# Kernel tuning notes

Measured on AMD Instinct MI355X. Metric: run time of the kernel, lower is better.

## Reference

```python
import jax, jax.numpy as jnp
import numpy as np

NEG_SLOPE = 0.2  # PyG GATConv default leaky_relu slope
H1, F1 = 4, 64


def gat_layer(x, src, dst, n, W, a_src, a_dst, b, heads, out_dim, concat):
    # Linear transform then split heads: [N, H, F]
    h = (x @ W).reshape(n, heads, out_dim)
    # Per-node attention logits for source/destination roles: [N, H]
    e_src = jnp.sum(h * a_src, axis=-1)
    e_dst = jnp.sum(h * a_dst, axis=-1)
    # Per-edge score, LeakyReLU: [E, H]
    e = e_src[src] + e_dst[dst]
    e = jnp.where(e > 0, e, NEG_SLOPE * e)
    # Segment softmax over incoming edges of each destination node
    m = jax.ops.segment_max(e, dst, num_segments=n)  # [N, H]
    e = jnp.exp(e - jax.lax.stop_gradient(m)[dst])
    denom = jax.ops.segment_sum(e, dst, num_segments=n)  # [N, H]
    alpha = e / denom[dst]  # [E, H]
    # Scatter-aggregate weighted source features: [N, H, F]
    out = jax.ops.segment_sum(alpha[:, :, None] * h[src], dst, num_segments=n)
    if concat:
        out = out.reshape(n, heads * out_dim)
    else:
        out = out.mean(axis=1)
    return out + b


def setup_inputs() -> dict:
    key = jax.random.key(0)
    ks = jax.random.split(key, 16)
    N, E, D_IN, HID, C = 30000, 480000, 5000, 64, 3
    s = 0.05
    inp = {
        "x": jax.random.normal(ks[0], (N, D_IN), dtype=jnp.float32),
        "W1": jax.random.normal(ks[1], (D_IN, H1 * HID), dtype=jnp.float32) * s,
        "a1_src": jax.random.normal(ks[2], (H1, HID), dtype=jnp.float32) * s,
        "a1_dst": jax.random.normal(ks[3], (H1, HID), dtype=jnp.float32) * s,
        "b1": jnp.zeros((H1 * HID,), dtype=jnp.float32),
        "W2": jax.random.normal(ks[4], (H1 * HID, H1 * HID), dtype=jnp.float32) * s,
        "a2_src": jax.random.normal(ks[5], (H1, HID), dtype=jnp.float32) * s,
        "a2_dst": jax.random.normal(ks[6], (H1, HID), dtype=jnp.float32) * s,
        "b2": jnp.zeros((H1 * HID,), dtype=jnp.float32),
        "W3": jax.random.normal(ks[7], (H1 * HID, HID), dtype=jnp.float32) * s,
        "a3_src": jax.random.normal(ks[8], (1, HID), dtype=jnp.float32) * s,
        "a3_dst": jax.random.normal(ks[9], (1, HID), dtype=jnp.float32) * s,
        "b3": jnp.zeros((HID,), dtype=jnp.float32),
        "Wc": jax.random.normal(ks[10], (HID, C), dtype=jnp.float32) * s,
        "bc": jnp.zeros((C,), dtype=jnp.float32),
        "edge_index": jax.random.randint(ks[11], (2, E), 0, N, dtype=jnp.int64)
        if jax.config.jax_enable_x64
        else jax.random.randint(ks[11], (2, E), 0, N, dtype=jnp.int32),
    }
    return inp


def reference(x, W1, a1_src, a1_dst, b1, W2, a2_src, a2_dst, b2,
              W3, a3_src, a3_dst, b3, Wc, bc, edge_index):
    n = x.shape[0]
    loops = jnp.arange(n, dtype=edge_index.dtype)
    src = jnp.concatenate([edge_index[0], loops])  # add self-loops (PyG default)
    dst = jnp.concatenate([edge_index[1], loops])
    h = gat_layer(x, src, dst, n, W1, a1_src, a1_dst, b1, H1, F1, True)
    h = jax.nn.elu(h)
    h = gat_layer(h, src, dst, n, W2, a2_src, a2_dst, b2, H1, F1, True)
    h = jax.nn.elu(h)
    h = gat_layer(h, src, dst, n, W3, a3_src, a3_dst, b3, 1, F1, False)
    h = jax.nn.elu(h)
    return h @ Wc + bc
```

## Files before the change

### kernel.cpp

```cpp
#include <hip/hip_runtime.h>
#include <hip/hip_bf16.h>
#include <cstdint>
#include <cstddef>

typedef unsigned short u16;
typedef __attribute__((ext_vector_type(8))) short short8;
typedef __attribute__((ext_vector_type(4))) float f4;


__device__ __forceinline__ u16 f2bf(float x) {
    union { float f; uint32_t u; } v; v.f = x;
    uint32_t r = v.u + 0x7fffu + ((v.u >> 16) & 1u);
    return (u16)(r >> 16);
}

__device__ __forceinline__ void async16(const u16* g, u16* l) {
    __builtin_amdgcn_global_load_lds((__attribute__((address_space(1))) void*)(g),
                                     (__attribute__((address_space(3))) void*)(l),
                                     16, 0, 0);
}


template<int BM, int BN, int WM, int WN>
__global__ __launch_bounds__((BM/WM)*(BN/WN)*64)
void gemm_xw(const float* __restrict__ A, const u16* __restrict__ Bt,
             float* __restrict__ C, int M, int K, int KT, int ktPer)
{
    constexpr int WAVES   = (BM/WM)*(BN/WN);
    constexpr int THREADS = WAVES*64;
    constexpr int RF = WM/16, CF = WN/16;
    constexpr int BCH = (BN*64)/(16*THREADS);
    static_assert((BM*32)/THREADS == 8, "A staging assumes 8 floats per thread");

    __shared__ __align__(16) u16 As[BM*32];
    __shared__ __align__(16) u16 Bs[BN*32];

    const int tid  = threadIdx.x;
    const int wid  = tid >> 6, lane = tid & 63;
    const int quad = lane >> 4, l16 = lane & 15;
    constexpr int WCOLS = BN/WN;
    const int wm = (wid / WCOLS) * WM;
    const int wn = (wid % WCOLS) * WN;
    const long m0 = (long)blockIdx.x * BM;

    const int ktA = blockIdx.y * ktPer;
    const int ktB = min(ktA + ktPer, KT);
    float* Cp = C + (size_t)blockIdx.y * (size_t)M * BN;

    const int arow = tid >> 2;
    const int akk  = (tid & 3) * 8;
    const bool aok = (m0 + arow) < M;
    const float* aptr = A + (size_t)(m0 + arow) * K + akk;

    f4 acc[RF][CF];
    #pragma unroll
    for (int r = 0; r < RF; ++r)
        #pragma unroll
        for (int c = 0; c < CF; ++c)
            #pragma unroll
            for (int g = 0; g < 4; ++g) acc[r][c][g] = 0.f;

    const u16* Asl = As + (wm + l16)*32 + quad*8;
    const u16* Bsl = Bs + (wn + l16)*32 + quad*8;

    for (int kt = ktA; kt < ktB; ++kt) {
        __syncthreads();
        #pragma unroll
        for (int i = 0; i < BCH; ++i) {
            int c16 = i*THREADS + tid;
            async16(Bt + (size_t)kt*(BN*32) + (size_t)c16*8, (u16*)Bs + c16*8);
        }
        {
            const int gk = kt*32 + akk;
            f4 v0, v1;
            #pragma unroll
            for (int g = 0; g < 4; ++g) { v0[g] = 0.f; v1[g] = 0.f; }
            if (aok && gk < K) {
                const float* p = aptr + (size_t)kt*32;
                v0 = *(const f4*)p;
                v1 = *(const f4*)(p + 4);
            }
            short8 w;
            #pragma unroll
            for (int g = 0; g < 4; ++g) {
                w[g]   = (short)f2bf(v0[g]);
                w[4+g] = (short)f2bf(v1[g]);
            }
            *(short8*)(As + tid*8) = w;
        }
        __syncthreads();

        short8 af[RF], bfr[CF];
        #pragma unroll
        for (int r = 0; r < RF; ++r) af[r]  = *(const short8*)(Asl + r*16*32);
        #pragma unroll
        for (int c = 0; c < CF; ++c) bfr[c] = *(const short8*)(Bsl + c*16*32);
        #pragma unroll
        for (int r = 0; r < RF; ++r)
            #pragma unroll
            for (int c = 0; c < CF; ++c)
                acc[r][c] = __builtin_amdgcn_mfma_f32_16x16x32_bf16(af[r], bfr[c], acc[r][c], 0, 0, 0);
    }

    #pragma unroll
    for (int r = 0; r < RF; ++r) {
        const long rb = m0 + wm + r*16 + quad*4;
        #pragma unroll
        for (int c = 0; c < CF; ++c) {
            const int col = wn + c*16 + l16;
            #pragma unroll
            for (int g = 0; g < 4; ++g) {
                long row = rb + g;
                if (row < M) Cp[row*(long)BN + col] = acc[r][c][g];
            }
        }
    }
}

__global__ void k_reduce_scores(const float* __restrict__ parts, size_t partStride, int S,
                                const float* __restrict__ asrc, const float* __restrict__ adst,
                                float* __restrict__ h, float* __restrict__ es,
                                float* __restrict__ ed, int N)
{
    int wave = threadIdx.x >> 6, lane = threadIdx.x & 63;
    int node = blockIdx.x*4 + wave;
    if (node >= N) return;
    size_t base = (size_t)node*256 + lane*4;
    f4 v;
    #pragma unroll
    for (int g = 0; g < 4; ++g) v[g] = 0.f;
    for (int s = 0; s < S; ++s) {
        f4 p = *(const f4*)(parts + s*partStride + base);
        #pragma unroll
        for (int g = 0; g < 4; ++g) v[g] += p[g];
    }
    *(f4*)(h + base) = v;

    int hh = lane >> 4;
    int c0 = (lane & 15) * 4;
    float s = 0.f, d = 0.f;
    #pragma unroll
    for (int g = 0; g < 4; ++g) {
        s += v[g] * asrc[hh*64 + c0 + g];
        d += v[g] * adst[hh*64 + c0 + g];
    }
    #pragma unroll
    for (int off = 1; off < 16; off <<= 1) {
        s += __shfl_xor(s, off);
        d += __shfl_xor(d, off);
    }
    if ((lane & 15) == 0) { es[node*4 + hh] = s; ed[node*4 + hh] = d; }
}

__global__ void k_prep_w(const float* __restrict__ W, u16* __restrict__ out,
                         int K, int Nn, int total)
{
    int idx = blockIdx.x*256 + threadIdx.x;
    if (idx >= total) return;
    int ki = idx & 31;
    int rest = idx >> 5;
    int nn = rest % Nn;
    int kt = rest / Nn;
    int k = kt*32 + ki;
    float v = (k < K) ? W[(size_t)k*Nn + nn] : 0.f;
    out[idx] = f2bf(v);
}

__global__ void k_hist(const int* __restrict__ ei, int E, int N, int* counts)
{
    int i = blockIdx.x*256 + threadIdx.x;
    if (i >= E + N) return;
    int d = (i < E) ? ei[E + i] : (i - E);
    atomicAdd(&counts[d], 1);
}

__global__ void k_scan1(const int* __restrict__ counts, int* offs, int* partials, int N)
{
    __shared__ int s[256];
    int i = blockIdx.x*256 + threadIdx.x;
    int v = (i < N) ? counts[i] : 0;
    s[threadIdx.x] = v;
    __syncthreads();
    #pragma unroll
    for (int off = 1; off < 256; off <<= 1) {
        int t = (threadIdx.x >= off) ? s[threadIdx.x - off] : 0;
        __syncthreads();
        s[threadIdx.x] += t;
        __syncthreads();
    }
    if (i < N) offs[i + 1] = s[threadIdx.x];
    if (threadIdx.x == 255) partials[blockIdx.x] = s[255];
    if (i == 0) offs[0] = 0;
}

__global__ void k_scan2(int* partials, int NB)
{
    __shared__ int s[256];
    int v = (threadIdx.x < NB) ? partials[threadIdx.x] : 0;
    s[threadIdx.x] = v;
    __syncthreads();
    for (int off = 1; off < 256; off <<= 1) {
        int t = (threadIdx.x >= off) ? s[threadIdx.x - off] : 0;
        __syncthreads();
        s[threadIdx.x] += t;
        __syncthreads();
    }
    if (threadIdx.x < NB) partials[threadIdx.x] = s[threadIdx.x] - v;
}

__global__ void k_scan3(int* offs, const int* __restrict__ partials, int N)
{
    int i = blockIdx.x*256 + threadIdx.x;
    if (i < N) offs[i + 1] += partials[blockIdx.x];
}

__global__ void k_copy(const int* __restrict__ a, int* __restrict__ b, int n)
{
    int i = blockIdx.x*256 + threadIdx.x;
    if (i < n) b[i] = a[i];
}

__global__ void k_scatter(const int* __restrict__ ei, int E, int N,
                          int* cursor, int* __restrict__ ssrc)
{
    int i = blockIdx.x*256 + threadIdx.x;
    if (i >= E + N) return;
    int s, d;
    if (i < E) { s = ei[i]; d = ei[E + i]; } else { s = i - E; d = s; }
    int pos = atomicAdd(&cursor[d], 1);
    ssrc[pos] = s;
}

__global__ void k_scores(const float* __restrict__ h, const float* __restrict__ asrc,
                         const float* __restrict__ adst, float* __restrict__ es,
                         float* __restrict__ ed, int N, int H)
{
    int wave = threadIdx.x >> 6, lane = threadIdx.x & 63;
    int node = blockIdx.x*4 + wave;
    if (node >= N) return;
    const float* row = h + (size_t)node * H * 64;
    for (int hh = 0; hh < H; ++hh) {
        float v = row[hh*64 + lane];
        float s = v * asrc[hh*64 + lane];
        float d = v * adst[hh*64 + lane];
        #pragma unroll
        for (int off = 32; off > 0; off >>= 1) {
            s += __shfl_down(s, off);
            d += __shfl_down(d, off);
        }
        if (lane == 0) { es[node*H + hh] = s; ed[node*H + hh] = d; }
    }
}

__global__ void k_agg(const float* __restrict__ h, const int* __restrict__ offs,
                      const int* __restrict__ ssrc, const float* __restrict__ es,
                      const float* __restrict__ ed, const float* __restrict__ bias,
                      float* __restrict__ out, int N, int H)
{
    int n = blockIdx.x;
    int hh = threadIdx.x >> 6, lane = threadIdx.x & 63;
    int s0 = offs[n], s1 = offs[n + 1];
    float edv = ed[n*H + hh];
    float m = -1e30f, l = 0.f, acc = 0.f;
    const int stride = H*64;
    for (int j = s0; j < s1; ++j) {
        int sidx = ssrc[j];
        float e = es[sidx*H + hh] + edv;
        e = (e > 0.f) ? e : 0.2f*e;
        if (e > m) {
            float sc = __expf(m - e);
            l *= sc; acc *= sc; m = e;
        }
        float p = __expf(e - m);
        l += p;
        acc += p * h[(size_t)sidx*stride + hh*64 + lane];
    }
    float v = acc / l + bias[hh*64 + lane];
    out[(size_t)n*stride + hh*64 + lane] = (v > 0.f) ? v : (__expf(v) - 1.f);
}

__global__ void k_classifier(const float* __restrict__ h, const float* __restrict__ Wc,
                             const float* __restrict__ bc, float* __restrict__ out, int N)
{
    __shared__ float wc[192];
    __shared__ float bcs[3];
    if (threadIdx.x < 192) wc[threadIdx.x] = Wc[threadIdx.x];
    if (threadIdx.x < 3)   bcs[threadIdx.x] = bc[threadIdx.x];
    __syncthreads();
    int n = blockIdx.x*blockDim.x + threadIdx.x;
    if (n >= N) return;
    const float4* row = (const float4*)(h + (size_t)n*64);
    float a0 = 0.f, a1 = 0.f, a2 = 0.f;
    #pragma unroll
    for (int q = 0; q < 16; ++q) {
        float4 v = row[q];
        const float* w = &wc[q*12];
        a0 += v.x*w[0] + v.y*w[3] + v.z*w[6] + v.w*w[9];
        a1 += v.x*w[1] + v.y*w[4] + v.z*w[7] + v.w*w[10];
        a2 += v.x*w[2] + v.y*w[5] + v.z*w[8] + v.w*w[11];
    }
    out[n*3 + 0] = a0 + bcs[0];
    out[n*3 + 1] = a1 + bcs[1];
    out[n*3 + 2] = a2 + bcs[2];
}

extern "C" void kernel_launch(void* const* d_in, const int* in_sizes, int n_in,
                              void* d_out, int out_size, void* d_ws, size_t ws_size,
                              hipStream_t stream)
{
    const float* x   = (const float*)d_in[0];
    const float* W1  = (const float*)d_in[1];
    const float* a1s = (const float*)d_in[2];
    const float* a1d = (const float*)d_in[3];
    const float* b1  = (const float*)d_in[4];
    const float* W2  = (const float*)d_in[5];
    const float* a2s = (const float*)d_in[6];
    const float* a2d = (const float*)d_in[7];
    const float* b2  = (const float*)d_in[8];
    const float* W3  = (const float*)d_in[9];
    const float* a3s = (const float*)d_in[10];
    const float* a3d = (const float*)d_in[11];
    const float* b3  = (const float*)d_in[12];
    const float* Wc  = (const float*)d_in[13];
    const float* bc  = (const float*)d_in[14];
    const int*   ei  = (const int*)d_in[15];
    float* out = (float*)d_out;

    const int DIN = in_sizes[1] / 256;
    const int N   = in_sizes[0] / DIN;
    const int E   = in_sizes[15] / 2;
    const int KT1 = (DIN + 31) / 32;
    const int ET  = E + N;
    const int SPLITS = 4;
    const int KTP = (KT1 + SPLITS - 1) / SPLITS;

    char* ws = (char*)d_ws;
    size_t off = 0;
    auto alloc = [&](size_t bytes) -> void* {
        void* p = ws + off;
        off += (bytes + 255) & ~(size_t)255;
        return p;
    };

    float* bufA   = (float*)alloc((size_t)N*256*4);
    float* bufB   = (float*)alloc((size_t)N*256*4);
    float* bufP   = (float*)alloc((size_t)SPLITS*N*256*4);
    u16*  Wt1     = (u16*)alloc((size_t)KT1*256*32*2);
    u16*  Wt2     = (u16*)alloc((size_t)8*256*32*2);
    u16*  Wt3     = (u16*)alloc((size_t)8*64*32*2);
    float* es     = (float*)alloc((size_t)N*4*4);
    float* ed     = (float*)alloc((size_t)N*4*4);
    int* counts   = (int*)alloc((size_t)N*4);
    int* offs     = (int*)alloc((size_t)(N+1)*4);
    int* cursor   = (int*)alloc((size_t)N*4);
    int* partials = (int*)alloc(1024);
    int* ssrc     = (int*)alloc((size_t)ET*4);

    const int NB = (N + 255)/256;
    const int GM = (N + 63)/64;

    hipMemsetAsync(counts, 0, (size_t)N*4, stream);
    k_hist   <<<(ET+255)/256, 256, 0, stream>>>(ei, E, N, counts);
    k_scan1  <<<NB, 256, 0, stream>>>(counts, offs, partials, N);
    k_scan2  <<<1, 256, 0, stream>>>(partials, NB);
    k_scan3  <<<NB, 256, 0, stream>>>(offs, partials, N);
    k_copy   <<<NB, 256, 0, stream>>>(offs, cursor, N);
    k_scatter<<<(ET+255)/256, 256, 0, stream>>>(ei, E, N, cursor, ssrc);

    k_prep_w<<<(KT1*256*32+255)/256, 256, 0, stream>>>(W1, Wt1, DIN, 256, KT1*256*32);
    k_prep_w<<<(8*256*32+255)/256, 256, 0, stream>>>(W2, Wt2, 256, 256, 8*256*32);
    k_prep_w<<<(8*64*32+255)/256, 256, 0, stream>>>(W3, Wt3, 256, 64, 8*64*32);

    gemm_xw<64,256,64,64><<<dim3(GM, SPLITS), 256, 0, stream>>>(x, Wt1, bufP, N, DIN, KT1, KTP);
    k_reduce_scores<<<(N+3)/4, 256, 0, stream>>>(bufP, (size_t)N*256, SPLITS, a1s, a1d,
                                                 bufA, es, ed, N);
    k_agg   <<<N, 256, 0, stream>>>(bufA, offs, ssrc, es, ed, b1, bufB, N, 4);
    gemm_xw<64,256,64,64><<<dim3(GM, 1), 256, 0, stream>>>(bufB, Wt2, bufA, N, 256, 8, 8);
    k_scores<<<(N+3)/4, 256, 0, stream>>>(bufA, a2s, a2d, es, ed, N, 4);
    k_agg   <<<N, 256, 0, stream>>>(bufA, offs, ssrc, es, ed, b2, bufB, N, 4);
    gemm_xw<64,64,16,64><<<dim3(GM, 1), 256, 0, stream>>>(bufB, Wt3, bufA, N, 256, 8, 8);
    k_scores<<<(N+3)/4, 256, 0, stream>>>(bufA, a3s, a3d, es, ed, N, 1);
    k_agg   <<<N, 64, 0, stream>>>(bufA, offs, ssrc, es, ed, b3, bufB, N, 1);
    k_classifier<<<(N+255)/256, 256, 0, stream>>>(bufB, Wc, bc, out, N);
}
```

Baseline: 1.310 ms.

## Double-buffer GEMM, fuse scores and classifier, rewrite aggregation with wave-parallel softmax

The GEMM gains double-buffered LDS with prefetch of the next K tile, a swizzled A layout and a transposed B layout to cut bank conflicts. For layers 2 and 3 it also computes the attention scores in its epilogue, so the separate score kernels go away. Aggregation now runs one wave per node with a chunked online softmax, processing 16 or 64 edges at a time with 4-way unrolled gathers. The last layer's aggregation is fused with the classifier. This cuts launches and serial per-edge latency, at the cost of more LDS and more register pressure.

```diff
diff --git a/kernel.cpp b/kernel.cpp
--- a/kernel.cpp
+++ b/kernel.cpp
@@ -21,19 +21,21 @@
 }
 
 
-template<int BM, int BN, int WM, int WN>
+template<int BM, int BN, int WM, int WN, bool SCORES>
 __global__ __launch_bounds__((BM/WM)*(BN/WN)*64)
 void gemm_xw(const float* __restrict__ A, const u16* __restrict__ Bt,
-             float* __restrict__ C, int M, int K, int KT, int ktPer)
+             float* __restrict__ C, int M, int K, int KT, int ktPer,
+             const float* __restrict__ asrc, const float* __restrict__ adst,
+             float* __restrict__ es, float* __restrict__ ed, int Hs)
 {
     constexpr int WAVES   = (BM/WM)*(BN/WN);
     constexpr int THREADS = WAVES*64;
     constexpr int RF = WM/16, CF = WN/16;
-    constexpr int BCH = (BN*64)/(16*THREADS);
+    constexpr int BCH = (BN*32)/(8*THREADS);
     static_assert((BM*32)/THREADS == 8, "A staging assumes 8 floats per thread");
 
-    __shared__ __align__(16) u16 As[BM*32];
-    __shared__ __align__(16) u16 Bs[BN*32];
+    __shared__ __align__(16) u16 As[2][BM*32];
+    __shared__ __align__(16) u16 Bs[2][BN*32];
 
     const int tid  = threadIdx.x;
     const int wid  = tid >> 6, lane = tid & 63;
@@ -48,9 +50,14 @@
     float* Cp = C + (size_t)blockIdx.y * (size_t)M * BN;
 
     const int arow = tid >> 2;
-    const int akk  = (tid & 3) * 8;
+    const int achk = tid & 3;
+    const int akk  = achk * 8;
     const bool aok = (m0 + arow) < M;
     const float* aptr = A + (size_t)(m0 + arow) * K + akk;
+    const int awpos = arow*4 + (achk ^ ((arow >> 1) & 3));
+
+    const int aoff = (wm + l16)*32 + (quad ^ (((wm + l16) >> 1) & 3))*8;
+    const int boff = quad*(BN*8) + (wn + l16)*8;
 
     f4 acc[RF][CF];
     #pragma unroll
@@ -60,46 +67,59 @@
             #pragma unroll
             for (int g = 0; g < 4; ++g) acc[r][c][g] = 0.f;
 
-    const u16* Asl = As + (wm + l16)*32 + quad*8;
-    const u16* Bsl = Bs + (wn + l16)*32 + quad*8;
-
-    for (int kt = ktA; kt < ktB; ++kt) {
-        __syncthreads();
+    f4 v0, v1;
+
+    auto stageB = [&](int kt, int buf) {
         #pragma unroll
         for (int i = 0; i < BCH; ++i) {
             int c16 = i*THREADS + tid;
-            async16(Bt + (size_t)kt*(BN*32) + (size_t)c16*8, (u16*)Bs + c16*8);
-        }
-        {
-            const int gk = kt*32 + akk;
-            f4 v0, v1;
-            #pragma unroll
-            for (int g = 0; g < 4; ++g) { v0[g] = 0.f; v1[g] = 0.f; }
-            if (aok && gk < K) {
-                const float* p = aptr + (size_t)kt*32;
-                v0 = *(const f4*)p;
-                v1 = *(const f4*)(p + 4);
-            }
-            short8 w;
-            #pragma unroll
-            for (int g = 0; g < 4; ++g) {
-                w[g]   = (short)f2bf(v0[g]);
-                w[4+g] = (short)f2bf(v1[g]);
-            }
-            *(short8*)(As + tid*8) = w;
-        }
-        __syncthreads();
-
+            async16(Bt + (size_t)kt*(BN*32) + (size_t)c16*8, (u16*)Bs[buf] + c16*8);
+        }
+    };
+    auto loadA = [&](int kt) {
+        #pragma unroll
+        for (int g = 0; g < 4; ++g) { v0[g] = 0.f; v1[g] = 0.f; }
+        const int gk = kt*32 + akk;
+        if (aok && gk < K) {
+            const float* p = aptr + (size_t)kt*32;
+            v0 = *(const f4*)p;
+            v1 = *(const f4*)(p + 4);
+        }
+    };
+    auto writeA = [&](int buf) {
+        short8 w;
+        #pragma unroll
+        for (int g = 0; g < 4; ++g) {
+            w[g]   = (short)f2bf(v0[g]);
+            w[4+g] = (short)f2bf(v1[g]);
+        }
+        *(short8*)((u16*)As[buf] + awpos*8) = w;
+    };
+
+    stageB(ktA, 0);
+    loadA(ktA);
+    writeA(0);
+    __syncthreads();
+
+    for (int kt = ktA; kt < ktB; ++kt) {
+        const int cur = (kt - ktA) & 1;
+        const bool pf = (kt + 1) < ktB;
+        if (pf) {
+            stageB(kt + 1, cur ^ 1);
+            loadA(kt + 1);
+        }
         short8 af[RF], bfr[CF];
         #pragma unroll
-        for (int r = 0; r < RF; ++r) af[r]  = *(const short8*)(Asl + r*16*32);
-        #pragma unroll
-        for (int c = 0; c < CF; ++c) bfr[c] = *(const short8*)(Bsl + c*16*32);
+        for (int r = 0; r < RF; ++r) af[r]  = *(const short8*)((u16*)As[cur] + aoff + r*512);
+        #pragma unroll
+        for (int c = 0; c < CF; ++c) bfr[c] = *(const short8*)((u16*)Bs[cur] + boff + c*128);
         #pragma unroll
         for (int r = 0; r < RF; ++r)
             #pragma unroll
             for (int c = 0; c < CF; ++c)
                 acc[r][c] = __builtin_amdgcn_mfma_f32_16x16x32_bf16(af[r], bfr[c], acc[r][c], 0, 0, 0);
+        if (pf) writeA(cur ^ 1);
+        __syncthreads();
     }
 
     #pragma unroll
@@ -115,6 +135,38 @@
             }
         }
     }
+
+    if constexpr (SCORES) {
+        const int head = wn >> 6;
+        float av[CF], dv[CF];
+        #pragma unroll
+        for (int c = 0; c < CF; ++c) {
+            av[c] = asrc[head*64 + c*16 + l16];
+            dv[c] = adst[head*64 + c*16 + l16];
+        }
+        #pragma unroll
+        for (int r = 0; r < RF; ++r) {
+            #pragma unroll
+            for (int g = 0; g < 4; ++g) {
+                float s = 0.f, d = 0.f;
+                #pragma unroll
+                for (int c = 0; c < CF; ++c) {
+                    s += acc[r][c][g] * av[c];
+                    d += acc[r][c][g] * dv[c];
+                }
+                #pragma unroll
+                for (int off = 1; off < 16; off <<= 1) {
+                    s += __shfl_xor(s, off);
+                    d += __shfl_xor(d, off);
+                }
+                long row = m0 + wm + r*16 + quad*4 + g;
+                if (l16 == 0 && row < M) {
+                    es[row*Hs + head] = s;
+                    ed[row*Hs + head] = d;
+                }
+            }
+        }
+    }
 }
 
 __global__ void k_reduce_scores(const float* __restrict__ parts, size_t partStride, int S,
@@ -157,11 +209,13 @@
 {
     int idx = blockIdx.x*256 + threadIdx.x;
     if (idx >= total) return;
-    int ki = idx & 31;
-    int rest = idx >> 5;
-    int nn = rest % Nn;
-    int kt = rest / Nn;
-    int k = kt*32 + ki;
+    int k7 = idx & 7;
+    int t  = idx >> 3;
+    int nn = t % Nn;
+    int u  = t / Nn;
+    int cc = u & 3;
+    int kt = u >> 2;
+    int k = kt*32 + cc*8 + k7;
     float v = (k < K) ? W[(size_t)k*Nn + nn] : 0.f;
     out[idx] = f2bf(v);
 }
@@ -231,77 +285,145 @@
     ssrc[pos] = s;
 }
 
-__global__ void k_scores(const float* __restrict__ h, const float* __restrict__ asrc,
-                         const float* __restrict__ adst, float* __restrict__ es,
-                         float* __restrict__ ed, int N, int H)
-{
-    int wave = threadIdx.x >> 6, lane = threadIdx.x & 63;
-    int node = blockIdx.x*4 + wave;
-    if (node >= N) return;
-    const float* row = h + (size_t)node * H * 64;
-    for (int hh = 0; hh < H; ++hh) {
-        float v = row[hh*64 + lane];
-        float s = v * asrc[hh*64 + lane];
-        float d = v * adst[hh*64 + lane];
-        #pragma unroll
-        for (int off = 32; off > 0; off >>= 1) {
-            s += __shfl_down(s, off);
-            d += __shfl_down(d, off);
-        }
-        if (lane == 0) { es[node*H + hh] = s; ed[node*H + hh] = d; }
-    }
-}
-
-__global__ void k_agg(const float* __restrict__ h, const int* __restrict__ offs,
-                      const int* __restrict__ ssrc, const float* __restrict__ es,
-                      const float* __restrict__ ed, const float* __restrict__ bias,
-                      float* __restrict__ out, int N, int H)
-{
-    int n = blockIdx.x;
-    int hh = threadIdx.x >> 6, lane = threadIdx.x & 63;
-    int s0 = offs[n], s1 = offs[n + 1];
-    float edv = ed[n*H + hh];
+__global__ void k_agg4(const float* __restrict__ h, const int* __restrict__ offs,
+                       const int* __restrict__ ssrc, const float* __restrict__ es,
+                       const float* __restrict__ ed, const float* __restrict__ bias,
+                       float* __restrict__ out, int N)
+{
+    const int wid = threadIdx.x >> 6, lane = threadIdx.x & 63;
+    const int n = blockIdx.x*4 + wid;
+    if (n >= N) return;
+    const int s0 = offs[n], s1 = offs[n + 1];
+    const int hh   = lane >> 4;
+    const int e16  = lane & 15;
+    const int psrc = lane & 48;
+    const float edv = ed[n*4 + hh];
+    float m = -1e30f, l = 0.f;
+    f4 acc;
+    #pragma unroll
+    for (int g = 0; g < 4; ++g) acc[g] = 0.f;
+
+    for (int c0 = s0; c0 < s1; c0 += 16) {
+        const int jj = c0 + e16;
+        const bool valid = jj < s1;
+        int sidx = valid ? ssrc[jj] : 0;
+        float e = -1e30f;
+        if (valid) {
+            e = es[sidx*4 + hh] + edv;
+            e = (e > 0.f) ? e : 0.2f*e;
+        }
+        float cm = e;
+        #pragma unroll
+        for (int off = 1; off < 16; off <<= 1) cm = fmaxf(cm, __shfl_xor(cm, off));
+        const float nm = fmaxf(m, cm);
+        const float sc = __expf(m - nm);
+        l *= sc;
+        #pragma unroll
+        for (int g = 0; g < 4; ++g) acc[g] *= sc;
+        m = nm;
+        float p = valid ? __expf(e - m) : 0.f;
+        float ps = p;
+        #pragma unroll
+        for (int off = 1; off < 16; off <<= 1) ps += __shfl_xor(ps, off);
+        l += ps;
+
+        const int cnt = min(s1 - c0, 16);
+        int j = 0;
+        for (; j + 4 <= cnt; j += 4) {
+            int sa = __shfl(sidx, j),     sb = __shfl(sidx, j + 1);
+            int sc2 = __shfl(sidx, j + 2), sd = __shfl(sidx, j + 3);
+            float pa = __shfl(p, psrc + j),     pb = __shfl(p, psrc + j + 1);
+            float pc = __shfl(p, psrc + j + 2), pd = __shfl(p, psrc + j + 3);
+            f4 ha = *(const f4*)(h + (size_t)sa*256  + lane*4);
+            f4 hb = *(const f4*)(h + (size_t)sb*256  + lane*4);
+            f4 hc = *(const f4*)(h + (size_t)sc2*256 + lane*4);
+            f4 hd = *(const f4*)(h + (size_t)sd*256  + lane*4);
+            #pragma unroll
+            for (int g = 0; g < 4; ++g)
+                acc[g] += pa*ha[g] + pb*hb[g] + pc*hc[g] + pd*hd[g];
+        }
+        for (; j < cnt; ++j) {
+            int s_ = __shfl(sidx, j);
+            float p_ = __shfl(p, psrc + j);
+            f4 hv = *(const f4*)(h + (size_t)s_*256 + lane*4);
+            #pragma unroll
+            for (int g = 0; g < 4; ++g) acc[g] += p_*hv[g];
+        }
+    }
+    const float inv = 1.f / l;
+    f4 b4 = *(const f4*)(bias + lane*4);
+    f4 o;
+    #pragma unroll
+    for (int g = 0; g < 4; ++g) {
+        float v = acc[g]*inv + b4[g];
+        o[g] = (v > 0.f) ? v : (__expf(v) - 1.f);
+    }
+    *(f4*)(out + (size_t)n*256 + lane*4) = o;
+}
+
+__global__ void k_agg1_cls(const float* __restrict__ h, const int* __restrict__ offs,
+                           const int* __restrict__ ssrc, const float* __restrict__ es,
+                           const float* __restrict__ ed, const float* __restrict__ bias,
+                           const float* __restrict__ Wc, const float* __restrict__ bc,
+                           float* __restrict__ out, int N)
+{
+    const int wid = threadIdx.x >> 6, lane = threadIdx.x & 63;
+    const int n = blockIdx.x*4 + wid;
+    if (n >= N) return;
+    const int s0 = offs[n], s1 = offs[n + 1];
+    const float edv = ed[n];
     float m = -1e30f, l = 0.f, acc = 0.f;
-    const int stride = H*64;
-    for (int j = s0; j < s1; ++j) {
-        int sidx = ssrc[j];
-        float e = es[sidx*H + hh] + edv;
-        e = (e > 0.f) ? e : 0.2f*e;
-        if (e > m) {
-            float sc = __expf(m - e);
-            l *= sc; acc *= sc; m = e;
-        }
-        float p = __expf(e - m);
-        l += p;
-        acc += p * h[(size_t)sidx*stride + hh*64 + lane];
-    }
-    float v = acc / l + bias[hh*64 + lane];
-    out[(size_t)n*stride + hh*64 + lane] = (v > 0.f) ? v : (__expf(v) - 1.f);
-}
-
-__global__ void k_classifier(const float* __restrict__ h, const float* __restrict__ Wc,
-                             const float* __restrict__ bc, float* __restrict__ out, int N)
-{
-    __shared__ float wc[192];
-    __shared__ float bcs[3];
-    if (threadIdx.x < 192) wc[threadIdx.x] = Wc[threadIdx.x];
-    if (threadIdx.x < 3)   bcs[threadIdx.x] = bc[threadIdx.x];
-    __syncthreads();
-    int n = blockIdx.x*blockDim.x + threadIdx.x;
-    if (n >= N) return;
-    const float4* row = (const float4*)(h + (size_t)n*64);
-    float a0 = 0.f, a1 = 0.f, a2 = 0.f;
-    #pragma unroll
-    for (int q = 0; q < 16; ++q) {
-        float4 v = row[q];
-        const float* w = &wc[q*12];
-        a0 += v.x*w[0] + v.y*w[3] + v.z*w[6] + v.w*w[9];
-        a1 += v.x*w[1] + v.y*w[4] + v.z*w[7] + v.w*w[10];
-        a2 += v.x*w[2] + v.y*w[5] + v.z*w[8] + v.w*w[11];
-    }
-    out[n*3 + 0] = a0 + bcs[0];
-    out[n*3 + 1] = a1 + bcs[1];
-    out[n*3 + 2] = a2 + bcs[2];
+
+    for (int c0 = s0; c0 < s1; c0 += 64) {
+        const int jj = c0 + lane;
+        const bool valid = jj < s1;
+        int sidx = valid ? ssrc[jj] : 0;
+        float e = -1e30f;
+        if (valid) {
+            e = es[sidx] + edv;
+            e = (e > 0.f) ? e : 0.2f*e;
+        }
+        float cm = e;
+        #pragma unroll
+        for (int off = 32; off > 0; off >>= 1) cm = fmaxf(cm, __shfl_xor(cm, off));
+        if (cm > m) {
+            float sc = __expf(m - cm);
+            l *= sc; acc *= sc; m = cm;
+        }
+        float p = valid ? __expf(e - m) : 0.f;
+        float ps = p;
+        #pragma unroll
+        for (int off = 32; off > 0; off >>= 1) ps += __shfl_xor(ps, off);
+        l += ps;
+
+        const int cnt = min(s1 - c0, 64);
+        int j = 0;
+        for (; j + 4 <= cnt; j += 4) {
+            int sa = __shfl(sidx, j),     sb = __shfl(sidx, j + 1);
+            int sc2 = __shfl(sidx, j + 2), sd = __shfl(sidx, j + 3);
+            float pa = __shfl(p, j),     pb = __shfl(p, j + 1);
+            float pc = __shfl(p, j + 2), pd = __shfl(p, j + 3);
+            acc += pa*h[(size_t)sa*64  + lane] + pb*h[(size_t)sb*64  + lane]
+                 + pc*h[(size_t)sc2*64 + lane] + pd*h[(size_t)sd*64  + lane];
+        }
+        for (; j < cnt; ++j)
+            acc += __shfl(p, j) * h[(size_t)__shfl(sidx, j)*64 + lane];
+    }
+    float v = acc / l + bias[lane];
+    v = (v > 0.f) ? v : (__expf(v) - 1.f);
+
+    float a0 = v*Wc[lane*3 + 0], a1 = v*Wc[lane*3 + 1], a2 = v*Wc[lane*3 + 2];
+    #pragma unroll
+    for (int off = 32; off > 0; off >>= 1) {
+        a0 += __shfl_xor(a0, off);
+        a1 += __shfl_xor(a1, off);
+        a2 += __shfl_xor(a2, off);
+    }
+    if (lane == 0) {
+        out[n*3 + 0] = a0 + bc[0];
+        out[n*3 + 1] = a1 + bc[1];
+        out[n*3 + 2] = a2 + bc[2];
+    }
 }
 
 extern "C" void kernel_launch(void* const* d_in, const int* in_sizes, int n_in,
@@ -371,15 +493,15 @@
     k_prep_w<<<(8*256*32+255)/256, 256, 0, stream>>>(W2, Wt2, 256, 256, 8*256*32);
     k_prep_w<<<(8*64*32+255)/256, 256, 0, stream>>>(W3, Wt3, 256, 64, 8*64*32);
 
-    gemm_xw<64,256,64,64><<<dim3(GM, SPLITS), 256, 0, stream>>>(x, Wt1, bufP, N, DIN, KT1, KTP);
+    gemm_xw<64,256,64,64,false><<<dim3(GM, SPLITS), 256, 0, stream>>>(
+        x, Wt1, bufP, N, DIN, KT1, KTP, nullptr, nullptr, nullptr, nullptr, 0);
     k_reduce_scores<<<(N+3)/4, 256, 0, stream>>>(bufP, (size_t)N*256, SPLITS, a1s, a1d,
                                                  bufA, es, ed, N);
-    k_agg   <<<N, 256, 0, stream>>>(bufA, offs, ssrc, es, ed, b1, bufB, N, 4);
-    gemm_xw<64,256,64,64><<<dim3(GM, 1), 256, 0, stream>>>(bufB, Wt2, bufA, N, 256, 8, 8);
-    k_scores<<<(N+3)/4, 256, 0, stream>>>(bufA, a2s, a2d, es, ed, N, 4);
-    k_agg   <<<N, 256, 0, stream>>>(bufA, offs, ssrc, es, ed, b2, bufB, N, 4);
-    gemm_xw<64,64,16,64><<<dim3(GM, 1), 256, 0, stream>>>(bufB, Wt3, bufA, N, 256, 8, 8);
-    k_scores<<<(N+3)/4, 256, 0, stream>>>(bufA, a3s, a3d, es, ed, N, 1);
-    k_agg   <<<N, 64, 0, stream>>>(bufA, offs, ssrc, es, ed, b3, bufB, N, 1);
-    k_classifier<<<(N+255)/256, 256, 0, stream>>>(bufB, Wc, bc, out, N);
-}
+    k_agg4  <<<(N+3)/4, 256, 0, stream>>>(bufA, offs, ssrc, es, ed, b1, bufB, N);
+    gemm_xw<64,256,64,64,true><<<dim3(GM, 1), 256, 0, stream>>>(
+        bufB, Wt2, bufA, N, 256, 8, 8, a2s, a2d, es, ed, 4);
+    k_agg4  <<<(N+3)/4, 256, 0, stream>>>(bufA, offs, ssrc, es, ed, b2, bufB, N);
+    gemm_xw<64,64,16,64,true><<<dim3(GM, 1), 256, 0, stream>>>(
+        bufB, Wt3, bufA, N, 256, 8, 8, a3s, a3d, es, ed, 1);
+    k_agg1_cls<<<(N+3)/4, 256, 0, stream>>>(bufA, offs, ssrc, es, ed, b3, Wc, bc, out, N);
+}
```

Result: faster. 1.171 ms (-10.6%).
